# Optimization experiments

Hardware: AMD Instinct MI355X
Metric: run time of the kernel (lower is better)

## Reference

```python
import jax, jax.numpy as jnp
import numpy as np

NF = 2560          # number of pyramid filters
TW = 16            # filter_temporal_width
H = W = 96
B, T = 8, 240
# center_idx = ceil(TW/2)-1 = 7 -> pad_left = TW-1-7 = 8, pad_right = 7
PAD_L, PAD_R = 8, 7
EPS = 1e-5
MASK_KEEP = 0.35   # approximate Gabor support fraction


def setup_inputs() -> dict:
    key = jax.random.key(0)
    ks = jax.random.split(key, 6)
    x = jax.random.normal(ks[0], (B, T, H, W), dtype=jnp.float32)
    w_s_sin = jax.random.normal(ks[1], (NF, H, W), dtype=jnp.float32)
    w_s_cos = jax.random.normal(ks[2], (NF, H, W), dtype=jnp.float32)
    # emulate the Gabor support mask (weights zeroed outside support)
    mask = (jax.random.uniform(ks[3], (NF, H, W)) < MASK_KEEP).astype(jnp.float32)
    w_s_sin = w_s_sin * mask
    w_s_cos = w_s_cos * mask
    w_t_sin = jax.random.normal(ks[4], (NF, TW), dtype=jnp.float32)
    w_t_cos = jax.random.normal(ks[5], (NF, TW), dtype=jnp.float32)
    return {"x": x, "w_s_sin": w_s_sin, "w_s_cos": w_s_cos,
            "w_t_sin": w_t_sin, "w_t_cos": w_t_cos}


def _dwconv1d(g, w):
    # g: (B, NF, T); w: (NF, TW) already time-flipped (cross-correlation),
    # depthwise conv with groups = NF, 'same'-style asymmetric padding.
    return jax.lax.conv_general_dilated(
        g, w[:, None, :], window_strides=(1,), padding=[(PAD_L, PAD_R)],
        dimension_numbers=("NCH", "OIH", "NCH"), feature_group_count=NF)


def reference(x, w_s_sin, w_s_cos, w_t_sin, w_t_cos):
    # full-frame spatial conv2d == contraction over (H, W): (B,T,NF)
    g_sin = jnp.einsum("bthw,fhw->bft", x, w_s_sin)  # (B, NF, T)
    g_cos = jnp.einsum("bthw,fhw->bft", x, w_s_cos)
    term1 = _dwconv1d(g_sin, w_t_cos)
    term2 = _dwconv1d(g_cos, w_t_sin)
    term3 = _dwconv1d(g_cos, w_t_cos)
    term4 = _dwconv1d(g_sin, w_t_sin)
    resp_sin = term1 + term2
    resp_cos = term3 - term4
    energy = jnp.log(jnp.sqrt(resp_sin * resp_sin + resp_cos * resp_cos) + EPS)
    return jnp.transpose(energy, (0, 2, 1))  # (B, T, NF)
```

## Files before the change

### kernel.cpp

```cpp
#include <hip/hip_runtime.h>

#define T_LEN   240
#define B_SZ    8
#define NFILT   2560
#define KD      9216
#define M_DIM   1920
#define N_DIM   5120
#define PAD_L   8
#define KSPLIT  3
#define KSLICE  3072
#define NT      96
#define GEMM_LDS 131072

typedef unsigned short u16;
typedef __attribute__((ext_vector_type(8)))  __bf16 bf16x8;
typedef __attribute__((ext_vector_type(16))) float  f32x16;

__device__ __forceinline__ u16 f2bf_rne(float f) {
    unsigned u = __float_as_uint(f);
    u += 0x7FFFu + ((u >> 16) & 1u);
    return (u16)(u >> 16);
}

__device__ __forceinline__ void split4(const float* __restrict__ src,
                                       u16* __restrict__ hi, u16* __restrict__ lo, int i) {
    const float4 v = ((const float4*)src)[i];
    float vv[4] = {v.x, v.y, v.z, v.w};
    u16 hh[4], ll[4];
#pragma unroll
    for (int j = 0; j < 4; ++j) {
        unsigned u = __float_as_uint(vv[j]);
        unsigned r = u + 0x7FFFu + ((u >> 16) & 1u);
        u16 hb = (u16)(r >> 16);
        float hf = __uint_as_float((unsigned)hb << 16);
        hh[j] = hb;
        ll[j] = f2bf_rne(vv[j] - hf);
    }
    ushort4 h, l;
    h.x = hh[0]; h.y = hh[1]; h.z = hh[2]; h.w = hh[3];
    l.x = ll[0]; l.y = ll[1]; l.z = ll[2]; l.w = ll[3];
    ((ushort4*)hi)[i] = h;
    ((ushort4*)lo)[i] = l;
}

#define NX4  (17694720 / 4)
#define NW4  (23592960 / 4)
#define NG4  (9830400 / 4)
__global__ void split_all_kernel(const float* __restrict__ x,
                                 const float* __restrict__ wss,
                                 const float* __restrict__ wsc,
                                 u16* __restrict__ xh, u16* __restrict__ xl,
                                 u16* __restrict__ wh, u16* __restrict__ wl,
                                 float* __restrict__ g) {
    int i = blockIdx.x * 256 + threadIdx.x;
    if (i < NX4) {
        split4(x, xh, xl, i);
    } else if (i < NX4 + NW4) {
        split4(wss, wh, wl, i - NX4);
    } else if (i < NX4 + 2 * NW4) {
        int j = i - NX4 - NW4;
        split4(wsc, wh + (size_t)NFILT * KD, wl + (size_t)NFILT * KD, j);
    }
    if (i < NG4) {
        float4 z; z.x = 0.f; z.y = 0.f; z.z = 0.f; z.w = 0.f;
        ((float4*)g)[i] = z;
    }
}

__device__ __forceinline__ void glds16(const u16* gp, __bf16* lp) {
    __builtin_amdgcn_global_load_lds(
        (const __attribute__((address_space(1))) void*)gp,
        (__attribute__((address_space(3))) void*)lp, 16, 0, 0);
}

__device__ __forceinline__ int frag_off(int r, int fo) {
    return r * 32 + (((fo >> 3) ^ ((r >> 1) & 3)) << 3);
}

__global__ __launch_bounds__(512, 2) void gemm_split_kernel(
    const u16* __restrict__ xh, const u16* __restrict__ xl,
    const u16* __restrict__ wh, const u16* __restrict__ wl,
    float* __restrict__ g) {

    extern __shared__ char smem_c[];
    __bf16* const smem = (__bf16*)smem_c;

    const int tid = threadIdx.x;
    const int l   = tid & 63;
    const int w   = tid >> 6;

    int bid = (int)blockIdx.x;
    bid = (bid & 7) * (160 * KSPLIT / 8) + (bid >> 3);
    const int ks = bid / 160;
    const int t  = bid % 160;
    const int m0 = (t / 20) * 256;
    const int n0 = (t % 20) * 256;
    const unsigned kb = (unsigned)ks * KSLICE;
    const bool mhalf = (m0 + 128 >= M_DIM);

    const int rl  = w * 16 + (l >> 2);
    const int gsw = ((l & 3) ^ ((rl >> 1) & 3)) * 8;
    const int sd  = w * 512 + l * 8;

    int ar0 = m0 + rl;        if (ar0 > M_DIM - 1) ar0 = M_DIM - 1;
    int ar1 = m0 + rl + 128;  if (ar1 > M_DIM - 1) ar1 = M_DIM - 1;
    const unsigned offA0 = (unsigned)ar0 * KD + kb + gsw;
    const unsigned offA1 = (unsigned)ar1 * KD + kb + gsw;
    const unsigned offB0 = (unsigned)(n0 + rl) * KD + kb + gsw;
    const unsigned offB1 = (unsigned)(n0 + rl + 128) * KD + kb + gsw;

#define ST_BH(D,KO) do { __bf16* s_ = smem + (D)*32768;                 \
        glds16(wh + (offB0 + (KO)), s_ + 16384 + sd);                   \
        glds16(wh + (offB1 + (KO)), s_ + 20480 + sd); } while (0)
#define ST_BL(D,KO) do { __bf16* s_ = smem + (D)*32768;                 \
        glds16(wl + (offB0 + (KO)), s_ + 24576 + sd);                   \
        glds16(wl + (offB1 + (KO)), s_ + 28672 + sd); } while (0)
#define ST_A0(D,KO) do { __bf16* s_ = smem + (D)*32768;                 \
        glds16(xh + (offA0 + (KO)), s_ + 0     + sd);                   \
        glds16(xl + (offA0 + (KO)), s_ + 8192  + sd); } while (0)
#define ST_A1(D,KO) do { __bf16* s_ = smem + (D)*32768;                 \
        glds16(xh + (offA1 + (KO)), s_ + 4096  + sd);                   \
        glds16(xl + (offA1 + (KO)), s_ + 12288 + sd); } while (0)

    const int rA = l & 31;
    const int kq = (l >> 5) * 8;
    const int wr = w >> 2;
    const int wc = w & 3;

    int aoff[2][2][2], boff[2][2];
#pragma unroll
    for (int h = 0; h < 2; ++h)
#pragma unroll
        for (int mf = 0; mf < 2; ++mf)
#pragma unroll
            for (int s = 0; s < 2; ++s)
                aoff[h][mf][s] = frag_off(h * 128 + wr * 64 + mf * 32 + rA, s * 16 + kq);
#pragma unroll
    for (int nf = 0; nf < 2; ++nf)
#pragma unroll
        for (int s = 0; s < 2; ++s)
            boff[nf][s] = frag_off(wc * 64 + nf * 32 + rA, s * 16 + kq);

    f32x16 acc[4][2];
#pragma unroll
    for (int i = 0; i < 4; ++i)
#pragma unroll
        for (int j = 0; j < 2; ++j)
#pragma unroll
            for (int r = 0; r < 16; ++r)
                acc[i][j][r] = 0.f;

#define MFMA3(ACC, AH, AL, BH, BL)                                              \
    ACC = __builtin_amdgcn_mfma_f32_32x32x16_bf16(AH, BH, ACC, 0, 0, 0);        \
    ACC = __builtin_amdgcn_mfma_f32_32x32x16_bf16(AH, BL, ACC, 0, 0, 0);        \
    ACC = __builtin_amdgcn_mfma_f32_32x32x16_bf16(AL, BH, ACC, 0, 0, 0);

    ST_BH(0, 0); ST_BL(0, 0); ST_A0(0, 0); ST_A1(0, 0);
    asm volatile("s_waitcnt vmcnt(2)" ::: "memory");
    __builtin_amdgcn_s_barrier();

    for (int kt = 0; kt < NT; ++kt) {
        const int cur = kt & 1;
        const int nxt = cur ^ 1;
        const __bf16* sb = smem + cur * 32768;
        const int ko = (kt + 1) * 32;
        const bool pf = (kt < NT - 1);

        bf16x8 bh_[2][2], bl_[2][2], ah_[2][2], al_[2][2];

        if (pf) { ST_BH(nxt, ko); ST_BL(nxt, ko); }
#pragma unroll
        for (int s = 0; s < 2; ++s) {
#pragma unroll
            for (int nf = 0; nf < 2; ++nf) {
                bh_[nf][s] = *(const bf16x8*)(sb + 16384 + boff[nf][s]);
                bl_[nf][s] = *(const bf16x8*)(sb + 24576 + boff[nf][s]);
            }
#pragma unroll
            for (int mf = 0; mf < 2; ++mf) {
                ah_[mf][s] = *(const bf16x8*)(sb + aoff[0][mf][s]);
                al_[mf][s] = *(const bf16x8*)(sb + 8192 + aoff[0][mf][s]);
            }
        }
        __builtin_amdgcn_s_setprio(1);
#pragma unroll
        for (int s = 0; s < 2; ++s)
#pragma unroll
            for (int mf = 0; mf < 2; ++mf)
#pragma unroll
                for (int nf = 0; nf < 2; ++nf) {
                    MFMA3(acc[mf][nf], ah_[mf][s], al_[mf][s], bh_[nf][s], bl_[nf][s]);
                }
        __builtin_amdgcn_s_setprio(0);
        if (pf) { asm volatile("s_waitcnt vmcnt(4)" ::: "memory"); }
        else    { asm volatile("s_waitcnt vmcnt(0)" ::: "memory"); }
        __builtin_amdgcn_s_barrier();

        if (pf) { ST_A0(nxt, ko); ST_A1(nxt, ko); }
        if (!mhalf) {
#pragma unroll
            for (int s = 0; s < 2; ++s)
#pragma unroll
                for (int mf = 0; mf < 2; ++mf) {
                    ah_[mf][s] = *(const bf16x8*)(sb + aoff[1][mf][s]);
                    al_[mf][s] = *(const bf16x8*)(sb + 8192 + aoff[1][mf][s]);
                }
            __builtin_amdgcn_s_setprio(1);
#pragma unroll
            for (int s = 0; s < 2; ++s)
#pragma unroll
                for (int mf = 0; mf < 2; ++mf)
#pragma unroll
                    for (int nf = 0; nf < 2; ++nf) {
                        MFMA3(acc[2 + mf][nf], ah_[mf][s], al_[mf][s], bh_[nf][s], bl_[nf][s]);
                    }
            __builtin_amdgcn_s_setprio(0);
        }
        if (pf) { asm volatile("s_waitcnt vmcnt(2)" ::: "memory"); }
        __builtin_amdgcn_s_barrier();
    }

    const int cb = (l >> 5) * 4;
    const int cc = l & 31;
#pragma unroll
    for (int am = 0; am < 4; ++am) {
        const int rowb = m0 + (am >> 1) * 128 + wr * 64 + (am & 1) * 32;
        if (rowb < M_DIM) {
#pragma unroll
            for (int nf = 0; nf < 2; ++nf) {
                const int col = n0 + wc * 64 + nf * 32 + cc;
                float* gp = g + (size_t)rowb * N_DIM + col;
#pragma unroll
                for (int r = 0; r < 16; ++r) {
                    const int ro = (r & 3) + 8 * (r >> 2) + cb;
                    atomicAdd(gp + (size_t)ro * N_DIM, acc[am][nf][r]);
                }
            }
        }
    }
#undef ST_BH
#undef ST_BL
#undef ST_A0
#undef ST_A1
#undef MFMA3
}

__global__ __launch_bounds__(256) void conv_energy_kernel(
    const float* __restrict__ g,
    const float* __restrict__ wts,
    const float* __restrict__ wtc,
    float* __restrict__ out) {

    __shared__ float wl_c[16][256];
    __shared__ float wl_s[16][256];

    const int tid = threadIdx.x;
    const int bid = blockIdx.x;
    const int fc  = bid % 10;
    const int t   = (bid / 10) % T_LEN;
    const int b   = bid / (10 * T_LEN);
    const int f0  = fc * 256;

    {
        const float4* wrc = (const float4*)(wtc + (size_t)(f0 + tid) * 16);
        const float4* wrs = (const float4*)(wts + (size_t)(f0 + tid) * 16);
#pragma unroll
        for (int k4 = 0; k4 < 4; ++k4) {
            const float4 vc = wrc[k4];
            const float4 vs = wrs[k4];
            wl_c[k4 * 4 + 0][tid] = vc.x; wl_c[k4 * 4 + 1][tid] = vc.y;
            wl_c[k4 * 4 + 2][tid] = vc.z; wl_c[k4 * 4 + 3][tid] = vc.w;
            wl_s[k4 * 4 + 0][tid] = vs.x; wl_s[k4 * 4 + 1][tid] = vs.y;
            wl_s[k4 * 4 + 2][tid] = vs.z; wl_s[k4 * 4 + 3][tid] = vs.w;
        }
    }
    __syncthreads();

    const float* grow = g + (size_t)b * T_LEN * N_DIM + f0 + tid;
    float s = 0.f, c = 0.f;
#pragma unroll
    for (int j = 0; j < 16; ++j) {
        const int tt = t + j - PAD_L;
        if (tt >= 0 && tt < T_LEN) {
            const float gs = grow[(size_t)tt * N_DIM];
            const float gc = grow[(size_t)tt * N_DIM + NFILT];
            const float a  = wl_c[j][tid];
            const float bb = wl_s[j][tid];
            s += gs * a + gc * bb;
            c += gc * a - gs * bb;
        }
    }
    const float r = sqrtf(s * s + c * c);
    out[(size_t)((b * T_LEN + t) * NFILT) + f0 + tid] = logf(r + 1e-5f);
}

extern "C" void kernel_launch(void* const* d_in, const int* in_sizes, int n_in,
                              void* d_out, int out_size, void* d_ws, size_t ws_size,
                              hipStream_t stream) {
    const float* x   = (const float*)d_in[0];
    const float* wss = (const float*)d_in[1];
    const float* wsc = (const float*)d_in[2];
    const float* wts = (const float*)d_in[3];
    const float* wtc = (const float*)d_in[4];
    float* out = (float*)d_out;

    char* ws = (char*)d_ws;
    u16*   xh  = (u16*)(ws);
    u16*   xl  = (u16*)(ws + 35389440);
    u16*   whi = (u16*)(ws + 70778880);
    u16*   wlo = (u16*)(ws + 165150720);
    float* g   = (float*)(ws + 259522560);

    static bool gemm_attr_set = false;
    if (!gemm_attr_set) {
        hipFuncSetAttribute(reinterpret_cast<const void*>(gemm_split_kernel),
                            hipFuncAttributeMaxDynamicSharedMemorySize, GEMM_LDS);
        gemm_attr_set = true;
    }

    const int ntot4 = NX4 + 2 * NW4;
    split_all_kernel<<<(ntot4 + 255) / 256, 256, 0, stream>>>(x, wss, wsc, xh, xl, whi, wlo, g);

    gemm_split_kernel<<<160 * KSPLIT, 512, GEMM_LDS, stream>>>(xh, xl, whi, wlo, g);

    conv_energy_kernel<<<B_SZ * T_LEN * 10, 256, 0, stream>>>(g, wts, wtc, out);
}
```

Baseline: 879.8 us.

## Software-pipeline GEMM LDS fragment reads and tile conv over 8 timesteps

```diff
diff --git a/kernel.cpp b/kernel.cpp
--- a/kernel.cpp
+++ b/kernel.cpp
@@ -127,14 +127,12 @@
     const int wr = w >> 2;
     const int wc = w & 3;
 
-    int aoff[2][2][2], boff[2][2];
-#pragma unroll
-    for (int h = 0; h < 2; ++h)
-#pragma unroll
-        for (int mf = 0; mf < 2; ++mf)
-#pragma unroll
-            for (int s = 0; s < 2; ++s)
-                aoff[h][mf][s] = frag_off(h * 128 + wr * 64 + mf * 32 + rA, s * 16 + kq);
+    int aoff[2][2], boff[2][2];
+#pragma unroll
+    for (int mf = 0; mf < 2; ++mf)
+#pragma unroll
+        for (int s = 0; s < 2; ++s)
+            aoff[mf][s] = frag_off(wr * 64 + mf * 32 + rA, s * 16 + kq);
 #pragma unroll
     for (int nf = 0; nf < 2; ++nf)
 #pragma unroll
@@ -149,75 +147,77 @@
 #pragma unroll
             for (int r = 0; r < 16; ++r)
                 acc[i][j][r] = 0.f;
+
+    bf16x8 bh0[2], bl0[2], bh1[2], bl1[2];
+    bf16x8 aXh[2], aXl[2], aYh[2], aYl[2];
+
+#define RD_B(SB, S, H, L) do {                                          \
+        H[0] = *(const bf16x8*)((SB) + 16384 + boff[0][S]);             \
+        H[1] = *(const bf16x8*)((SB) + 16384 + boff[1][S]);             \
+        L[0] = *(const bf16x8*)((SB) + 24576 + boff[0][S]);             \
+        L[1] = *(const bf16x8*)((SB) + 24576 + boff[1][S]); } while (0)
+#define RD_A(SB, HOFF, S, H, L) do {                                    \
+        H[0] = *(const bf16x8*)((SB) + (HOFF) + aoff[0][S]);            \
+        H[1] = *(const bf16x8*)((SB) + (HOFF) + aoff[1][S]);            \
+        L[0] = *(const bf16x8*)((SB) + 8192 + (HOFF) + aoff[0][S]);     \
+        L[1] = *(const bf16x8*)((SB) + 8192 + (HOFF) + aoff[1][S]); } while (0)
 
 #define MFMA3(ACC, AH, AL, BH, BL)                                              \
     ACC = __builtin_amdgcn_mfma_f32_32x32x16_bf16(AH, BH, ACC, 0, 0, 0);        \
     ACC = __builtin_amdgcn_mfma_f32_32x32x16_bf16(AH, BL, ACC, 0, 0, 0);        \
     ACC = __builtin_amdgcn_mfma_f32_32x32x16_bf16(AL, BH, ACC, 0, 0, 0);
 
+#define CLUSTER(AM, AH, AL, BH, BL) do {                                        \
+        __builtin_amdgcn_s_setprio(1);                                          \
+        MFMA3(acc[(AM) + 0][0], AH[0], AL[0], BH[0], BL[0]);                    \
+        MFMA3(acc[(AM) + 0][1], AH[0], AL[0], BH[1], BL[1]);                    \
+        MFMA3(acc[(AM) + 1][0], AH[1], AL[1], BH[0], BL[0]);                    \
+        MFMA3(acc[(AM) + 1][1], AH[1], AL[1], BH[1], BL[1]);                    \
+        __builtin_amdgcn_s_setprio(0);                                          \
+    } while (0)
+
     ST_BH(0, 0); ST_BL(0, 0); ST_A0(0, 0); ST_A1(0, 0);
     asm volatile("s_waitcnt vmcnt(2)" ::: "memory");
     __builtin_amdgcn_s_barrier();
+    RD_B(smem, 0, bh0, bl0);
+    RD_A(smem, 0, 0, aXh, aXl);
 
     for (int kt = 0; kt < NT; ++kt) {
         const int cur = kt & 1;
-        const int nxt = cur ^ 1;
         const __bf16* sb = smem + cur * 32768;
+        const __bf16* sn = smem + (cur ^ 1) * 32768;
         const int ko = (kt + 1) * 32;
         const bool pf = (kt < NT - 1);
 
-        bf16x8 bh_[2][2], bl_[2][2], ah_[2][2], al_[2][2];
-
-        if (pf) { ST_BH(nxt, ko); ST_BL(nxt, ko); }
-#pragma unroll
-        for (int s = 0; s < 2; ++s) {
-#pragma unroll
-            for (int nf = 0; nf < 2; ++nf) {
-                bh_[nf][s] = *(const bf16x8*)(sb + 16384 + boff[nf][s]);
-                bl_[nf][s] = *(const bf16x8*)(sb + 24576 + boff[nf][s]);
-            }
-#pragma unroll
-            for (int mf = 0; mf < 2; ++mf) {
-                ah_[mf][s] = *(const bf16x8*)(sb + aoff[0][mf][s]);
-                al_[mf][s] = *(const bf16x8*)(sb + 8192 + aoff[0][mf][s]);
-            }
-        }
-        __builtin_amdgcn_s_setprio(1);
-#pragma unroll
-        for (int s = 0; s < 2; ++s)
-#pragma unroll
-            for (int mf = 0; mf < 2; ++mf)
-#pragma unroll
-                for (int nf = 0; nf < 2; ++nf) {
-                    MFMA3(acc[mf][nf], ah_[mf][s], al_[mf][s], bh_[nf][s], bl_[nf][s]);
-                }
-        __builtin_amdgcn_s_setprio(0);
+        if (pf) { ST_BH(cur ^ 1, ko); ST_BL(cur ^ 1, ko); }
+        RD_B(sb, 1, bh1, bl1);
+        RD_A(sb, 0, 1, aYh, aYl);
+        __builtin_amdgcn_sched_barrier(0);
+        CLUSTER(0, aXh, aXl, bh0, bl0);
+
         if (pf) { asm volatile("s_waitcnt vmcnt(4)" ::: "memory"); }
         else    { asm volatile("s_waitcnt vmcnt(0)" ::: "memory"); }
         __builtin_amdgcn_s_barrier();
 
-        if (pf) { ST_A0(nxt, ko); ST_A1(nxt, ko); }
+        if (pf) { ST_A0(cur ^ 1, ko); ST_A1(cur ^ 1, ko); }
+        if (!mhalf) RD_A(sb, 4096, 0, aXh, aXl);
+        __builtin_amdgcn_sched_barrier(0);
+        CLUSTER(0, aYh, aYl, bh1, bl1);
+
         if (!mhalf) {
-#pragma unroll
-            for (int s = 0; s < 2; ++s)
-#pragma unroll
-                for (int mf = 0; mf < 2; ++mf) {
-                    ah_[mf][s] = *(const bf16x8*)(sb + aoff[1][mf][s]);
-                    al_[mf][s] = *(const bf16x8*)(sb + 8192 + aoff[1][mf][s]);
-                }
-            __builtin_amdgcn_s_setprio(1);
-#pragma unroll
-            for (int s = 0; s < 2; ++s)
-#pragma unroll
-                for (int mf = 0; mf < 2; ++mf)
-#pragma unroll
-                    for (int nf = 0; nf < 2; ++nf) {
-                        MFMA3(acc[2 + mf][nf], ah_[mf][s], al_[mf][s], bh_[nf][s], bl_[nf][s]);
-                    }
-            __builtin_amdgcn_s_setprio(0);
-        }
-        if (pf) { asm volatile("s_waitcnt vmcnt(2)" ::: "memory"); }
-        __builtin_amdgcn_s_barrier();
+            RD_A(sb, 4096, 1, aYh, aYl);
+            __builtin_amdgcn_sched_barrier(0);
+            CLUSTER(2, aXh, aXl, bh0, bl0);
+        }
+
+        if (pf) {
+            asm volatile("s_waitcnt vmcnt(2)" ::: "memory");
+            __builtin_amdgcn_s_barrier();
+            RD_B(sn, 0, bh0, bl0);
+            RD_A(sn, 0, 0, aXh, aXl);
+            __builtin_amdgcn_sched_barrier(0);
+        }
+        if (!mhalf) CLUSTER(2, aYh, aYl, bh1, bl1);
     }
 
     const int cb = (l >> 5) * 4;
@@ -242,7 +242,10 @@
 #undef ST_BL
 #undef ST_A0
 #undef ST_A1
+#undef RD_B
+#undef RD_A
 #undef MFMA3
+#undef CLUSTER
 }
 
 __global__ __launch_bounds__(256) void conv_energy_kernel(
@@ -257,9 +260,10 @@
     const int tid = threadIdx.x;
     const int bid = blockIdx.x;
     const int fc  = bid % 10;
-    const int t   = (bid / 10) % T_LEN;
-    const int b   = bid / (10 * T_LEN);
+    const int t8  = (bid / 10) % 30;
+    const int b   = bid / 300;
     const int f0  = fc * 256;
+    const int t0  = t8 * 8;
 
     {
         const float4* wrc = (const float4*)(wtc + (size_t)(f0 + tid) * 16);
@@ -277,21 +281,31 @@
     __syncthreads();
 
     const float* grow = g + (size_t)b * T_LEN * N_DIM + f0 + tid;
-    float s = 0.f, c = 0.f;
-#pragma unroll
-    for (int j = 0; j < 16; ++j) {
-        const int tt = t + j - PAD_L;
+    float gsv[23], gcv[23];
+#pragma unroll
+    for (int r = 0; r < 23; ++r) {
+        const int tt = t0 + r - PAD_L;
         if (tt >= 0 && tt < T_LEN) {
-            const float gs = grow[(size_t)tt * N_DIM];
-            const float gc = grow[(size_t)tt * N_DIM + NFILT];
+            gsv[r] = grow[(size_t)tt * N_DIM];
+            gcv[r] = grow[(size_t)tt * N_DIM + NFILT];
+        } else {
+            gsv[r] = 0.f; gcv[r] = 0.f;
+        }
+    }
+
+    float* orow = out + (size_t)((b * T_LEN + t0) * NFILT) + f0 + tid;
+#pragma unroll
+    for (int tt = 0; tt < 8; ++tt) {
+        float s = 0.f, c = 0.f;
+#pragma unroll
+        for (int j = 0; j < 16; ++j) {
             const float a  = wl_c[j][tid];
             const float bb = wl_s[j][tid];
-            s += gs * a + gc * bb;
-            c += gc * a - gs * bb;
-        }
-    }
-    const float r = sqrtf(s * s + c * c);
-    out[(size_t)((b * T_LEN + t) * NFILT) + f0 + tid] = logf(r + 1e-5f);
+            s += gsv[tt + j] * a + gcv[tt + j] * bb;
+            c += gcv[tt + j] * a - gsv[tt + j] * bb;
+        }
+        orow[(size_t)tt * NFILT] = logf(sqrtf(s * s + c * c) + 1e-5f);
+    }
 }
 
 extern "C" void kernel_launch(void* const* d_in, const int* in_sizes, int n_in,
@@ -323,5 +337,5 @@
 
     gemm_split_kernel<<<160 * KSPLIT, 512, GEMM_LDS, stream>>>(xh, xl, whi, wlo, g);
 
-    conv_energy_kernel<<<B_SZ * T_LEN * 10, 256, 0, stream>>>(g, wts, wtc, out);
-}
+    conv_energy_kernel<<<B_SZ * 30 * 10, 256, 0, stream>>>(g, wts, wtc, out);
+}
```

Result: faster. 778.1 us (-11.6%).
